# Kernel optimization log

Measured on AMD Instinct MI355X. Metric: run time of the kernel, lower is better.

Reference implementation:

```python
import jax, jax.numpy as jnp
import numpy as np

IN_SIZE = 4096   # input_size
OUT_SIZE = 4096  # output_size
RANK = 1024      # len(S_4), multiple of 32
GROUPSIZE = 128
BITS = 4
PACK = 32 // BITS  # 8 nibbles per int32
MAXQ_MASK = (1 << BITS) - 1  # 15


def _dequant4(qweight, qzeros, scales, g_idx):
    """GPTQ 4-bit dequant. qweight: int32 [K//8, N]; qzeros: int32 [G, N//8];
    scales: [G, N]; g_idx: int32 [K]. Returns W [K, N] with
    W[k, n] = (int4[k, n] - (zero4[g_idx[k], n] + 1)) * scales[g_idx[k], n]."""
    shifts = (jnp.arange(PACK, dtype=jnp.int32) * BITS)
    K = qweight.shape[0] * PACK
    N = qweight.shape[1]
    # unpack along rows: [K//8, 8, N] -> [K, N]
    intw = ((qweight[:, None, :] >> shifts[None, :, None]) & MAXQ_MASK).reshape(K, N)
    # unpack along cols: [G, N//8, 8] -> [G, N]; pack() stored zeros-1, so add 1 back
    zeros = ((qzeros[:, :, None] >> shifts[None, None, :]) & MAXQ_MASK).reshape(qzeros.shape[0], N) + 1
    sc = scales[g_idx]            # [K, N]
    zr = zeros[g_idx].astype(scales.dtype)  # [K, N]
    return (intw.astype(scales.dtype) - zr) * sc


def setup_inputs() -> dict:
    key = jax.random.key(0)
    ks = jax.random.split(key, 9)
    qweight_V = jax.random.randint(ks[0], (IN_SIZE // PACK, RANK), 0, 2**31 - 1, dtype=jnp.int32)
    qzeros_V = jax.random.randint(ks[1], (IN_SIZE // GROUPSIZE, RANK // PACK), 0, 2**31 - 1, dtype=jnp.int32)
    scales_V = jax.random.uniform(ks[2], (IN_SIZE // GROUPSIZE, RANK), dtype=jnp.float32) * 0.01 + 1e-3
    g_idx_V = (jnp.arange(IN_SIZE, dtype=jnp.int32) // GROUPSIZE).astype(jnp.int32)
    qweight_U = jax.random.randint(ks[3], (RANK // PACK, OUT_SIZE), 0, 2**31 - 1, dtype=jnp.int32)
    qzeros_U = jax.random.randint(ks[4], (RANK // GROUPSIZE, OUT_SIZE // PACK), 0, 2**31 - 1, dtype=jnp.int32)
    scales_U = jax.random.uniform(ks[5], (RANK // GROUPSIZE, OUT_SIZE), dtype=jnp.float32) * 0.01 + 1e-3
    g_idx_U = (jnp.arange(RANK, dtype=jnp.int32) // GROUPSIZE).astype(jnp.int32)
    S = jax.random.uniform(ks[6], (RANK,), dtype=jnp.float32) + 0.1  # singular values
    x = jax.random.normal(ks[7], (4, 2048, IN_SIZE), dtype=jnp.float32)
    return {"x": x,
            "qweight_V": qweight_V, "qzeros_V": qzeros_V, "scales_V": scales_V, "g_idx_V": g_idx_V,
            "qweight_U": qweight_U, "qzeros_U": qzeros_U, "scales_U": scales_U, "g_idx_U": g_idx_U,
            "S": S}


def reference(x, qweight_V, qzeros_V, scales_V, g_idx_V,
              qweight_U, qzeros_U, scales_U, g_idx_U, S):
    # weight_V: dequantized [IN_SIZE, RANK]; weight_U: dequantized [RANK, OUT_SIZE]
    weight_V = _dequant4(qweight_V, qzeros_V, scales_V, g_idx_V)
    weight_U = _dequant4(qweight_U, qzeros_U, scales_U, g_idx_U)
    # forward returns (weight_V @ diag(S) @ weight_U).T  -> [OUT_SIZE, IN_SIZE]
    # (the x @ W_V @ diag(S) @ W_U activation path in the source is dead code
    #  w.r.t. the returned value)
    return ((weight_V * S[None, :]) @ weight_U).T
```

## Files before the change

kernel.cpp:

```cpp
#include <hip/hip_runtime.h>

typedef __attribute__((ext_vector_type(8))) short bf16x8;
typedef __attribute__((ext_vector_type(4))) float f32x4;
typedef __attribute__((ext_vector_type(16))) float f32x16;

__device__ __forceinline__ short f2bf(float f) {
  unsigned u = __builtin_bit_cast(unsigned, f);
  u += 0x7fffu + ((u >> 16) & 1u);
  return (short)(u >> 16);
}


__global__ __launch_bounds__(256) void dequant_fused(
    const int* __restrict__ qw_V, const int* __restrict__ qz_V,
    const float* __restrict__ sc_V, const float* __restrict__ S,
    short* __restrict__ A,
    const int* __restrict__ qw_U, const int* __restrict__ qz_U,
    const float* __restrict__ sc_U, short* __restrict__ B) {
  const int bid = blockIdx.x;
  if (bid < 2048) {
    const int t    = bid * 256 + threadIdx.x;
    const int tile = t >> 9;
    const int blk  = (t >> 6) & 7;
    const int lane = t & 63;
    const int m  = (tile >> 5) * 128 + (blk >> 1) * 32 + (lane & 31);
    const int r0 = (tile & 31) * 32 + (blk & 1) * 16 + ((lane >> 5) << 3);
    const int g  = m >> 7;
    const int sh = (m & 7) << 2;
    const int zw = qz_V[(g << 7) + (r0 >> 3)];
    const int*   wq  = qw_V + (m >> 3) * 1024 + r0;
    const float* scp = sc_V + (g << 10) + r0;
    const float* sp  = S + r0;
    bf16x8 res;
#pragma unroll
    for (int e = 0; e < 8; ++e) {
      int q = (wq[e] >> sh) & 15;
      int z = ((zw >> (e << 2)) & 15) + 1;
      res[e] = f2bf((float)(q - z) * scp[e] * sp[e]);
    }
    *(bf16x8*)(A + ((size_t)t << 3)) = res;
  } else {
    const int t    = (bid - 2048) * 256 + threadIdx.x;
    const int tile = t >> 10;
    const int blk  = (t >> 6) & 15;
    const int lane = t & 63;
    const int n  = (tile >> 5) * 256 + (blk >> 1) * 32 + (lane & 31);
    const int r0 = (tile & 31) * 32 + (blk & 1) * 16 + ((lane >> 5) << 3);
    const int w  = qw_U[(r0 >> 3) * 4096 + n];
    const int g  = r0 >> 7;
    const int zw = qz_U[(g << 9) + (n >> 3)];
    const int z  = ((zw >> ((n & 7) << 2)) & 15) + 1;
    const float s = sc_U[(g << 12) + n];
    bf16x8 res;
#pragma unroll
    for (int e = 0; e < 8; ++e) {
      int q = (w >> (e << 2)) & 15;
      res[e] = f2bf((float)(q - z) * s);
    }
    *(bf16x8*)(B + ((size_t)t << 3)) = res;
  }
}

#define GLL(g, l)                                                              \
  __builtin_amdgcn_global_load_lds(                                            \
      (const __attribute__((address_space(1))) void*)(g),                      \
      (__attribute__((address_space(3))) void*)(l), 16, 0, 0)

__global__ __launch_bounds__(512, 4) void gemm128x256(
    const short* __restrict__ A, const short* __restrict__ B,
    float* __restrict__ out) {
  __shared__ __align__(16) char lds[49152];
  const int tid  = threadIdx.x;
  const int lane = tid & 63;
  const int wid  = tid >> 6;
  const int wm   = wid >> 2;
  const int wn   = wid & 3;
  const int bid = ((blockIdx.x & 7) << 6) | (blockIdx.x >> 3);
  const int mp = bid >> 4;
  const int np = bid & 15;

  const short* gAp = A + (size_t)mp * 131072 + tid * 8;
  const short* gBp = B + (size_t)np * 262144 + tid * 8;
  char* const ldsA = lds + (wid << 10);
  char* const ldsB = lds + 8192 + (wid << 10);

#define STAGE(kt) do {                                                         \
    const int bo_ = ((kt) & 1) * 24576;                                        \
    GLL(gAp + (size_t)(kt) * 4096,        ldsA + bo_);                         \
    GLL(gBp + (size_t)(kt) * 8192,        ldsB + bo_);                         \
    GLL(gBp + (size_t)(kt) * 8192 + 4096, ldsB + bo_ + 8192);                  \
  } while (0)

  const char* Ard = lds + (lane << 4);
  const char* Brd = lds + 8192 + (lane << 4);

  f32x16 acc[2][2];
#pragma unroll
  for (int i = 0; i < 2; ++i)
#pragma unroll
    for (int j = 0; j < 2; ++j)
#pragma unroll
      for (int e = 0; e < 16; ++e) acc[i][j][e] = 0.f;

  STAGE(0);
  STAGE(1);
  asm volatile("s_waitcnt vmcnt(3)" ::: "memory");
  __builtin_amdgcn_s_barrier();

  for (int kt = 0; kt < 32; ++kt) {
    const int bo = (kt & 1) * 24576;
    bf16x8 a[2][2], b[2][2];
#pragma unroll
    for (int mi2 = 0; mi2 < 2; ++mi2)
#pragma unroll
      for (int kk = 0; kk < 2; ++kk)
        a[mi2][kk] = *(const bf16x8*)(Ard + bo +
                       (((wm * 2 + mi2) * 2 + kk) << 10));
#pragma unroll
    for (int nj2 = 0; nj2 < 2; ++nj2)
#pragma unroll
      for (int kk = 0; kk < 2; ++kk)
        b[nj2][kk] = *(const bf16x8*)(Brd + bo +
                       (((wn * 2 + nj2) * 2 + kk) << 10));
    asm volatile("s_waitcnt lgkmcnt(0)" ::: "memory");
    __builtin_amdgcn_sched_barrier(0);
    __builtin_amdgcn_s_barrier();
    if (kt < 30) STAGE(kt + 2);
    __builtin_amdgcn_s_setprio(1);
#pragma unroll
    for (int kk = 0; kk < 2; ++kk)
#pragma unroll
      for (int mi2 = 0; mi2 < 2; ++mi2)
#pragma unroll
        for (int nj2 = 0; nj2 < 2; ++nj2)
          acc[mi2][nj2] = __builtin_amdgcn_mfma_f32_32x32x16_bf16(
              a[mi2][kk], b[nj2][kk], acc[mi2][nj2], 0, 0, 0);
    __builtin_amdgcn_s_setprio(0);
    if (kt < 30)       asm volatile("s_waitcnt vmcnt(3)" ::: "memory");
    else if (kt == 30) asm volatile("s_waitcnt vmcnt(0)" ::: "memory");
    if (kt < 31) __builtin_amdgcn_s_barrier();
  }

#pragma unroll
  for (int mi2 = 0; mi2 < 2; ++mi2)
#pragma unroll
    for (int nj2 = 0; nj2 < 2; ++nj2) {
      const int mb = mp * 128 + wm * 64 + mi2 * 32 + ((lane >> 5) << 2);
      const int nb = np * 256 + wn * 64 + nj2 * 32 + (lane & 31);
      const f32x16 c = acc[mi2][nj2];
#pragma unroll
      for (int q = 0; q < 4; ++q) {
        f32x4 v = {c[q * 4], c[q * 4 + 1], c[q * 4 + 2], c[q * 4 + 3]};
        *(f32x4*)(out + (size_t)nb * 4096 + mb + 8 * q) = v;
      }
    }
#undef STAGE
}

extern "C" void kernel_launch(void* const* d_in, const int* in_sizes, int n_in,
                              void* d_out, int out_size, void* d_ws, size_t ws_size,
                              hipStream_t stream) {
  const int*   qw_V = (const int*)d_in[1];
  const int*   qz_V = (const int*)d_in[2];
  const float* sc_V = (const float*)d_in[3];
  const int*   qw_U = (const int*)d_in[5];
  const int*   qz_U = (const int*)d_in[6];
  const float* sc_U = (const float*)d_in[7];
  const float* S    = (const float*)d_in[9];

  short* A = (short*)d_ws;
  short* B = (short*)d_ws + 4096 * 1024;
  float* out = (float*)d_out;

  dequant_fused<<<4096, 256, 0, stream>>>(qw_V, qz_V, sc_V, S, A,
                                          qw_U, qz_U, sc_U, B);
  gemm128x256<<<512, 512, 0, stream>>>(A, B, out);
}
```

Measured before the change: 56.79 us.

## Replace LDS-staged GEMM with direct global-to-register double-buffered loads

Drops the shared-memory staging (global_load_lds plus barriers) and has each wave load its MFMA operand fragments straight from global memory, which works because the dequant kernel already writes them in fragment-ready order. Register double buffering (a0/b0, a1/b1) overlaps loads with MFMAs. The block shrinks to 4 waves, each owning a 64x128 output tile instead of 64x64. The cost is that operands shared between waves are fetched repeatedly from L2 rather than once into LDS, and register pressure rises, which may lower occupancy.

```diff
diff --git a/kernel.cpp b/kernel.cpp
--- a/kernel.cpp
+++ b/kernel.cpp
@@ -61,100 +61,86 @@
   }
 }
 
-#define GLL(g, l)                                                              \
-  __builtin_amdgcn_global_load_lds(                                            \
-      (const __attribute__((address_space(1))) void*)(g),                      \
-      (__attribute__((address_space(3))) void*)(l), 16, 0, 0)
-
-__global__ __launch_bounds__(512, 4) void gemm128x256(
+__global__ __launch_bounds__(256, 2) void gemm_direct(
     const short* __restrict__ A, const short* __restrict__ B,
     float* __restrict__ out) {
-  __shared__ __align__(16) char lds[49152];
   const int tid  = threadIdx.x;
   const int lane = tid & 63;
   const int wid  = tid >> 6;
-  const int wm   = wid >> 2;
-  const int wn   = wid & 3;
+  const int wm   = wid >> 1;
+  const int wn   = wid & 1;
   const int bid = ((blockIdx.x & 7) << 6) | (blockIdx.x >> 3);
   const int mp = bid >> 4;
   const int np = bid & 15;
 
-  const short* gAp = A + (size_t)mp * 131072 + tid * 8;
-  const short* gBp = B + (size_t)np * 262144 + tid * 8;
-  char* const ldsA = lds + (wid << 10);
-  char* const ldsB = lds + 8192 + (wid << 10);
+  const short* Ab = A + ((size_t)(mp * 256 + wm * 4) << 9) + lane * 8;
+  const short* Bb = B + ((size_t)(np * 512 + wn * 8) << 9) + lane * 8;
 
-#define STAGE(kt) do {                                                         \
-    const int bo_ = ((kt) & 1) * 24576;                                        \
-    GLL(gAp + (size_t)(kt) * 4096,        ldsA + bo_);                         \
-    GLL(gBp + (size_t)(kt) * 8192,        ldsB + bo_);                         \
-    GLL(gBp + (size_t)(kt) * 8192 + 4096, ldsB + bo_ + 8192);                  \
-  } while (0)
-
-  const char* Ard = lds + (lane << 4);
-  const char* Brd = lds + 8192 + (lane << 4);
-
-  f32x16 acc[2][2];
+  f32x16 acc[2][4];
 #pragma unroll
   for (int i = 0; i < 2; ++i)
 #pragma unroll
-    for (int j = 0; j < 2; ++j)
+    for (int j = 0; j < 4; ++j)
 #pragma unroll
       for (int e = 0; e < 16; ++e) acc[i][j][e] = 0.f;
 
-  STAGE(0);
-  STAGE(1);
-  asm volatile("s_waitcnt vmcnt(3)" ::: "memory");
-  __builtin_amdgcn_s_barrier();
+  bf16x8 a0[2][2], b0[4][2], a1[2][2], b1[4][2];
 
-  for (int kt = 0; kt < 32; ++kt) {
-    const int bo = (kt & 1) * 24576;
-    bf16x8 a[2][2], b[2][2];
-#pragma unroll
-    for (int mi2 = 0; mi2 < 2; ++mi2)
-#pragma unroll
-      for (int kk = 0; kk < 2; ++kk)
-        a[mi2][kk] = *(const bf16x8*)(Ard + bo +
-                       (((wm * 2 + mi2) * 2 + kk) << 10));
-#pragma unroll
-    for (int nj2 = 0; nj2 < 2; ++nj2)
-#pragma unroll
-      for (int kk = 0; kk < 2; ++kk)
-        b[nj2][kk] = *(const bf16x8*)(Brd + bo +
-                       (((wn * 2 + nj2) * 2 + kk) << 10));
-    asm volatile("s_waitcnt lgkmcnt(0)" ::: "memory");
-    __builtin_amdgcn_sched_barrier(0);
-    __builtin_amdgcn_s_barrier();
-    if (kt < 30) STAGE(kt + 2);
-    __builtin_amdgcn_s_setprio(1);
-#pragma unroll
-    for (int kk = 0; kk < 2; ++kk)
-#pragma unroll
-      for (int mi2 = 0; mi2 < 2; ++mi2)
-#pragma unroll
-        for (int nj2 = 0; nj2 < 2; ++nj2)
-          acc[mi2][nj2] = __builtin_amdgcn_mfma_f32_32x32x16_bf16(
-              a[mi2][kk], b[nj2][kk], acc[mi2][nj2], 0, 0, 0);
-    __builtin_amdgcn_s_setprio(0);
-    if (kt < 30)       asm volatile("s_waitcnt vmcnt(3)" ::: "memory");
-    else if (kt == 30) asm volatile("s_waitcnt vmcnt(0)" ::: "memory");
-    if (kt < 31) __builtin_amdgcn_s_barrier();
+#define LDA(dst, kt) do {                                                      \
+    _Pragma("unroll")                                                          \
+    for (int mi = 0; mi < 2; ++mi)                                             \
+      _Pragma("unroll")                                                        \
+      for (int kk = 0; kk < 2; ++kk)                                           \
+        dst[mi][kk] = *(const bf16x8*)(Ab + (((kt) * 8 + mi * 2 + kk) << 9));  \
+  } while (0)
+#define LDB(dst, kt) do {                                                      \
+    _Pragma("unroll")                                                          \
+    for (int nj = 0; nj < 4; ++nj)                                             \
+      _Pragma("unroll")                                                        \
+      for (int kk = 0; kk < 2; ++kk)                                           \
+        dst[nj][kk] = *(const bf16x8*)(Bb + (((kt) * 16 + nj * 2 + kk) << 9)); \
+  } while (0)
+#define MM(aa, bb) do {                                                        \
+    __builtin_amdgcn_s_setprio(1);                                             \
+    _Pragma("unroll")                                                          \
+    for (int kk = 0; kk < 2; ++kk)                                             \
+      _Pragma("unroll")                                                        \
+      for (int mi = 0; mi < 2; ++mi)                                           \
+        _Pragma("unroll")                                                      \
+        for (int nj = 0; nj < 4; ++nj)                                         \
+          acc[mi][nj] = __builtin_amdgcn_mfma_f32_32x32x16_bf16(               \
+              aa[mi][kk], bb[nj][kk], acc[mi][nj], 0, 0, 0);                   \
+    __builtin_amdgcn_s_setprio(0);                                             \
+  } while (0)
+
+  LDA(a0, 0); LDB(b0, 0);
+
+  for (int kt = 0; kt < 30; kt += 2) {
+    LDA(a1, kt + 1); LDB(b1, kt + 1);
+    MM(a0, b0);
+    LDA(a0, kt + 2); LDB(b0, kt + 2);
+    MM(a1, b1);
   }
+  LDA(a1, 31); LDB(b1, 31);
+  MM(a0, b0);
+  MM(a1, b1);
 
 #pragma unroll
-  for (int mi2 = 0; mi2 < 2; ++mi2)
+  for (int mi = 0; mi < 2; ++mi)
 #pragma unroll
-    for (int nj2 = 0; nj2 < 2; ++nj2) {
-      const int mb = mp * 128 + wm * 64 + mi2 * 32 + ((lane >> 5) << 2);
-      const int nb = np * 256 + wn * 64 + nj2 * 32 + (lane & 31);
-      const f32x16 c = acc[mi2][nj2];
+    for (int nj = 0; nj < 4; ++nj) {
+      const int mb = mp * 128 + wm * 64 + mi * 32 + ((lane >> 5) << 2);
+      const int nb = np * 256 + wn * 128 + nj * 32 + (lane & 31);
+      const f32x16 c = acc[mi][nj];
 #pragma unroll
       for (int q = 0; q < 4; ++q) {
         f32x4 v = {c[q * 4], c[q * 4 + 1], c[q * 4 + 2], c[q * 4 + 3]};
         *(f32x4*)(out + (size_t)nb * 4096 + mb + 8 * q) = v;
       }
     }
-#undef STAGE
+#undef LDA
+#undef LDB
+#undef MM
 }
 
 extern "C" void kernel_launch(void* const* d_in, const int* in_sizes, int n_in,
@@ -174,5 +160,5 @@
 
   dequant_fused<<<4096, 256, 0, stream>>>(qw_V, qz_V, sc_V, S, A,
                                           qw_U, qz_U, sc_U, B);
-  gemm128x256<<<512, 512, 0, stream>>>(A, B, out);
+  gemm_direct<<<512, 256, 0, stream>>>(A, B, out);
 }
```

Result: slower. 64.30 us (+13.2%).
